# Optimization experiments

Measured on AMD Instinct MI355X. Metric: run time of the kernel, lower is better.

Reference implementation:

```python
import jax, jax.numpy as jnp
import numpy as np

B = 2048
NUM_GENES = 4096
# (stratum, n_terms, input_dim, output_dim, genes_per_term) leaves -> root
CFG = [(4, 256, 16, 20, 16), (3, 64, 144, 20, 64), (2, 16, 336, 77, 256), (1, 4, 1332, 308, 1024), (0, 1, 5328, 1229, 4096)]
EPS = 1e-5


def setup_inputs() -> dict:
    key = jax.random.key(0)
    ks = iter(jax.random.split(key, 64))
    inp = {"x": jax.random.uniform(next(ks), (B, NUM_GENES), dtype=jnp.float32)}
    sc = 0.05  # uniform init scale (original uses 0.001; scaled up for numerically robust baseline)
    for s, T, I, O, _ in CFG:
        inp[f"W{s}"] = jax.random.uniform(next(ks), (T, I, O), minval=-sc, maxval=sc, dtype=jnp.float32)
        inp[f"b{s}"] = jax.random.uniform(next(ks), (T, O), minval=-sc, maxval=sc, dtype=jnp.float32)
        inp[f"g{s}"] = jnp.ones((T, O), jnp.float32)   # BN weight
        inp[f"bb{s}"] = jnp.zeros((T, O), jnp.float32)  # BN bias
        inp[f"hw{s}"] = jax.random.uniform(next(ks), (T, O, 1), minval=-sc, maxval=sc, dtype=jnp.float32)
        inp[f"hb{s}"] = jnp.zeros((T, 1), jnp.float32)
    return inp


def _forward(x, W4, b4, g4, bb4, hw4, hb4, W3, b3, g3, bb3, hw3, hb3,
             W2, b2, g2, bb2, hw2, hb2, W1, b1, g1, bb1, hw1, hb1,
             W0, b0, g0, bb0, hw0, hb0):
    Bm = x.shape[0]
    params = [(W4, b4, g4, bb4, hw4, hb4), (W3, b3, g3, bb3, hw3, hb3),
              (W2, b2, g2, bb2, hw2, hb2), (W1, b1, g1, bb1, hw1, hb1),
              (W0, b0, g0, bb0, hw0, hb0)]
    act = None
    heads = []
    for (W, b, g, bb, hw, hb), (_, T, _, _, Gs) in zip(params, CFG):
        # gene states for each term: contiguous block gather == reshape
        genes = x.reshape(Bm, T, Gs)
        if act is None:
            inp = genes
        else:
            # concat 4 children outputs per parent, then gene states (children first, per _calculate_input_dim)
            inp = jnp.concatenate([act.reshape(Bm, T, -1), genes], axis=-1)
        # per-term Linear -> BatchNorm1d (training mode, biased var) -> Tanh, batched over terms
        h = jnp.einsum('bti,tio->bto', inp, W) + b
        mu = jnp.mean(h, axis=0)
        var = jnp.var(h, axis=0)
        act = jnp.tanh((h - mu) * jax.lax.rsqrt(var + EPS) * g + bb)
        # per-term linear head (output_size=1)
        heads.append(jnp.squeeze(jnp.einsum('bto,tos->bts', act, hw), -1) + hb[:, 0])
    # concat all per-term scalar outputs leaves->root; root prediction is heads[:, -1]
    return jnp.concatenate(heads, axis=1)


def reference(x, W4, b4, g4, bb4, hw4, hb4, W3, b3, g3, bb3, hw3, hb3,
              W2, b2, g2, bb2, hw2, hb2, W1, b1, g1, bb1, hw1, hb1,
              W0, b0, g0, bb0, hw0, hb0):
    return _forward(x, W4, b4, g4, bb4, hw4, hb4, W3, b3, g3, bb3, hw3, hb3,
                    W2, b2, g2, bb2, hw2, hb2, W1, b1, g1, bb1, hw1, hb1,
                    W0, b0, g0, bb0, hw0, hb0)
```

## Files before the change

### kernel.cpp

```cpp
#include <hip/hip_runtime.h>
#include <hip/hip_bf16.h>


#define BDIM 2048
#define OUTW 341

typedef __attribute__((ext_vector_type(8))) short short8;
typedef __attribute__((ext_vector_type(4))) float float4v;

static __device__ __forceinline__ unsigned short f2bf(float f) {
    union { float f; unsigned u; } c{f};
    unsigned r = c.u + 0x7FFF + ((c.u >> 16) & 1);
    return (unsigned short)(r >> 16);
}
static __device__ __forceinline__ float bf2f(unsigned short s) {
    union { unsigned u; float f; } c{(unsigned)s << 16};
    return c.f;
}

static __device__ __forceinline__ float fast_tanh(float x) {
    float ax = __builtin_fabsf(x);
    float e  = __builtin_amdgcn_exp2f(ax * 2.8853900817779268f);
    float r  = 1.f - 2.f * __builtin_amdgcn_rcpf(e + 1.f);
    return __builtin_copysignf(r, x);
}

static __device__ __forceinline__ void bn_ss(float sm, float sq, float g, float bb,
                                             float& scale, float& shift) {
    float mu = sm * (1.f / BDIM);
    float var = sq * (1.f / BDIM) - mu * mu;
    scale = rsqrtf(var + 1e-5f) * g;
    shift = bb - mu * scale;
}

static __device__ __forceinline__ void stage16(const void* g, void* ldsBase, int lane) {
#if __has_builtin(__builtin_amdgcn_global_load_lds)
    __builtin_amdgcn_global_load_lds(
        (const __attribute__((address_space(1))) unsigned int*)(uintptr_t)g,
        (__attribute__((address_space(3))) unsigned int*)(unsigned int)(uintptr_t)ldsBase,
        16, 0, 0);
#else
    *(uint4*)((char*)ldsBase + lane * 16) = *(const uint4*)g;
#endif
}

static __device__ __forceinline__ void cvt_w_body(const float* Wt, unsigned short* dst,
                                                  int I, int O, int Npad, int Kpad,
                                                  int i0, int o0, int tid) {
    __shared__ unsigned short tile[32][33];
    const int c = tid & 31, r0 = tid >> 5;
    #pragma unroll
    for (int rr = 0; rr < 4; rr++) {
        int i = i0 + r0 + rr * 8, o = o0 + c;
        float v = (i < I && o < O) ? Wt[(size_t)i * O + o] : 0.f;
        tile[r0 + rr * 8][c] = f2bf(v);
    }
    __syncthreads();
    #pragma unroll
    for (int rr = 0; rr < 4; rr++) {
        int o = o0 + r0 + rr * 8, k = i0 + c;
        if (o < Npad) dst[(size_t)o * Kpad + k] = tile[c][r0 + rr * 8];
    }
}

#define PACK_BLOCKS ((BDIM * 512 + BDIM * 24 + 255) / 256)
#define CVT_BLOCKS  2896
#define W0P1_BLOCKS (168 * 24)
__global__ __launch_bounds__(256) void pack_cvt(const float* __restrict__ x,
                                                unsigned short* __restrict__ ain0,
                                                unsigned short* __restrict__ ain1,
                                                const float* __restrict__ W4,
                                                const float* __restrict__ W3,
                                                const float* __restrict__ W2,
                                                const float* __restrict__ W1,
                                                const float* __restrict__ W0,
                                                unsigned short* __restrict__ wbt,
                                                float* __restrict__ acc) {
    int bid = blockIdx.x;
    if (bid < 20) {
        int idx = bid * 1024 + threadIdx.x * 4;
        *(float4*)(acc + idx) = make_float4(0.f, 0.f, 0.f, 0.f);
    }
    if (bid < PACK_BLOCKS) {
        const int MAIN = BDIM * 512;
        int i = bid * 256 + threadIdx.x;
        if (i < MAIN) {
            int b = i >> 9, j = i & 511;
            const float* xp = x + (size_t)b * 4096 + j * 8;
            float4 lo = *(const float4*)xp, hi = *(const float4*)(xp + 4);
            union { unsigned short u[8]; uint4 v4; uint2 v2[2]; } t;
            t.u[0] = f2bf(lo.x); t.u[1] = f2bf(lo.y); t.u[2] = f2bf(lo.z); t.u[3] = f2bf(lo.w);
            t.u[4] = f2bf(hi.x); t.u[5] = f2bf(hi.y); t.u[6] = f2bf(hi.z); t.u[7] = f2bf(hi.w);
            *(uint4*)(ain0 + (size_t)b * 5376 + 1232 + j * 8) = t.v4;
            int gi = j * 8, tt = gi >> 10, u = gi & 1023;
            unsigned short* d1 = ain1 + (size_t)b * 5376 + tt * 1344 + 308 + u;
            *(uint2*)d1 = t.v2[0];
            *(uint2*)(d1 + 4) = t.v2[1];
            return;
        }
        int zi = i - MAIN;
        const int ZU = BDIM * 12;
        if (zi < ZU) {
            int b = zi / 12, u = zi % 12;
            *(uint2*)(ain0 + (size_t)b * 5376 + 5328 + u * 4) = make_uint2(0u, 0u);
        } else if (zi < 2 * ZU) {
            zi -= ZU;
            int b = zi / 12, u = zi % 12, tt = u / 3, k = u % 3;
            *(uint2*)(ain1 + (size_t)b * 5376 + tt * 1344 + 1332 + k * 4) = make_uint2(0u, 0u);
        }
        return;
    }
    bid -= PACK_BLOCKS;
    if (bid >= CVT_BLOCKS) {
        bid -= CVT_BLOCKS;
        int bx = bid % 168, by = 16 + bid / 168;
        cvt_w_body(W0, wbt, 5328, 1229, 1280, 5376, bx * 32, by * 32, threadIdx.x);
        return;
    }
    const float* W; unsigned short* dst;
    int I, O, Npad, Kpad, gx, gy, local;
    if (bid < 256)       { W = W4; dst = wbt;           I = 16;   O = 20;  Npad = 20;  Kpad = 32;   gx = 1;  gy = 1;  local = bid; }
    else if (bid < 640)  { W = W3; dst = wbt + 163840;  I = 144;  O = 20;  Npad = 20;  Kpad = 192;  gx = 6;  gy = 1;  local = bid - 256; }
    else if (bid < 1216) { W = W2; dst = wbt + 409600;  I = 336;  O = 77;  Npad = 77;  Kpad = 384;  gx = 12; gy = 3;  local = bid - 640; }
    else                 { W = W1; dst = wbt + 882688;  I = 1332; O = 308; Npad = 320; Kpad = 1344; gx = 42; gy = 10; local = bid - 1216; }
    int per = gx * gy;
    int t = local / per, rem = local % per;
    int by = rem / gx, bx = rem % gx;
    cvt_w_body(W + (size_t)t * I * O, dst + (size_t)t * Npad * Kpad,
               I, O, Npad, Kpad, bx * 32, by * 32, threadIdx.x);
}

__global__ __launch_bounds__(256) void cvt_w(const float* __restrict__ W,
                                             unsigned short* __restrict__ WbT,
                                             int I, int O, int Npad, int Kpad) {
    cvt_w_body(W + (size_t)blockIdx.z * I * O, WbT + (size_t)blockIdx.z * Npad * Kpad,
               I, O, Npad, Kpad, blockIdx.x * 32, blockIdx.y * 32, threadIdx.x);
}

__global__ __launch_bounds__(256) void s4_stats(
    const unsigned short* __restrict__ xg,
    const unsigned short* __restrict__ wbt4,
    const float* __restrict__ b4,
    float* __restrict__ acc4)
{
    const int cg = blockIdx.x & 31;
    const int rc = blockIdx.x >> 5;
    const int t0 = cg * 8, b0 = rc * 64;
    const int tid = threadIdx.x;
    const int lane = tid & 63, w = tid >> 6;
    const int l15 = lane & 15, quad = lane >> 4;

    __shared__ __align__(16) unsigned short xs[64][168];

    #pragma unroll
    for (int j = 0; j < 4; j++) {
        int i = tid + j * 256;
        int r = i >> 4, gg = i & 15;
        *(uint4*)&xs[r][gg * 8] =
            *(const uint4*)(xg + (size_t)(b0 + r) * 5376 + t0 * 16 + gg * 8);
    }
    if (tid < 128) {
        int r = tid >> 1, gg = 16 + (tid & 1);
        *(uint4*)&xs[r][gg * 8] = make_uint4(0u, 0u, 0u, 0u);
    }
    __syncthreads();

    float4v acc[2][4][2];
    #pragma unroll
    for (int a = 0; a < 2; a++)
        #pragma unroll
        for (int b = 0; b < 4; b++)
            #pragma unroll
            for (int c = 0; c < 2; c++)
                acc[a][b][c] = (float4v){0.f, 0.f, 0.f, 0.f};

    #pragma unroll
    for (int ti = 0; ti < 2; ti++) {
        const int lt = w * 2 + ti;
        const int t = t0 + lt;
        short8 bf[2];
        #pragma unroll
        for (int nf = 0; nf < 2; nf++)
            bf[nf] = *(const short8*)(wbt4 + ((size_t)t * 20 + nf * 16 + l15) * 32 + quad * 8);
        #pragma unroll
        for (int mf = 0; mf < 4; mf++) {
            short8 a = *(const short8*)&xs[mf * 16 + l15][lt * 16 + quad * 8];
            #pragma unroll
            for (int nf = 0; nf < 2; nf++)
                acc[ti][mf][nf] = __builtin_amdgcn_mfma_f32_16x16x32_bf16(a, bf[nf], acc[ti][mf][nf], 0, 0, 0);
        }
    }

    #pragma unroll
    for (int ti = 0; ti < 2; ti++) {
        const int lt = w * 2 + ti;
        #pragma unroll
        for (int nf = 0; nf < 2; nf++) {
            const int o = nf * 16 + l15;
            const int col = (t0 + lt) * 20 + o;
            const bool valid = (o < 20);
            const float bias = valid ? b4[col] : 0.f;
            float s = 0.f, s2 = 0.f;
            #pragma unroll
            for (int mf = 0; mf < 4; mf++)
                #pragma unroll
                for (int r = 0; r < 4; r++) {
                    float v = acc[ti][mf][nf][r] + bias;
                    s += v; s2 += v * v;
                }
            s  += __shfl_xor(s, 16, 64);  s  += __shfl_xor(s, 32, 64);
            s2 += __shfl_xor(s2, 16, 64); s2 += __shfl_xor(s2, 32, 64);
            if (quad == 0 && valid) {
                atomicAdd(acc4 + col, s);
                atomicAdd(acc4 + 5120 + col, s2);
            }
        }
    }
}

__global__ __launch_bounds__(256) void s4s3_fused(
    const unsigned short* __restrict__ xg,
    const unsigned short* __restrict__ wbt4,
    const unsigned short* __restrict__ wbt3,
    const float* __restrict__ b4,
    const float* __restrict__ acc4,
    const float* __restrict__ g4,
    const float* __restrict__ bb4,
    const float* __restrict__ hw4,
    const float* __restrict__ hb4,
    const float* __restrict__ b3,
    unsigned short* __restrict__ h3,
    float* __restrict__ acc3,
    float* __restrict__ out)
{
    const int cg = blockIdx.x & 31;
    const int rc = blockIdx.x >> 5;
    const int t0 = cg * 8, b0 = rc * 64;
    const int tid = threadIdx.x;
    const int lane = tid & 63, w = tid >> 6;
    const int l15 = lane & 15, quad = lane >> 4;

    __shared__ __align__(16) unsigned short gs[64][152];
    __shared__ __align__(16) unsigned short as_[64][168];

    #pragma unroll
    for (int j = 0; j < 4; j++) {
        int i = tid + j * 256;
        int r = i >> 4, gg = i & 15;
        *(uint4*)&gs[r][gg * 8] =
            *(const uint4*)(xg + (size_t)(b0 + r) * 5376 + t0 * 16 + gg * 8);
    }
    if (tid < 128) {
        int r = tid >> 1, gg = 16 + (tid & 1);
        *(uint4*)&gs[r][gg * 8] = make_uint4(0u, 0u, 0u, 0u);
    }
    __syncthreads();

    float4v acc[2][4][2];
    #pragma unroll
    for (int a = 0; a < 2; a++)
        #pragma unroll
        for (int b = 0; b < 4; b++)
            #pragma unroll
            for (int c = 0; c < 2; c++)
                acc[a][b][c] = (float4v){0.f, 0.f, 0.f, 0.f};

    #pragma unroll
    for (int ti = 0; ti < 2; ti++) {
        const int lt = w * 2 + ti;
        const int t = t0 + lt;
        short8 bf[2];
        #pragma unroll
        for (int nf = 0; nf < 2; nf++)
            bf[nf] = *(const short8*)(wbt4 + ((size_t)t * 20 + nf * 16 + l15) * 32 + quad * 8);
        #pragma unroll
        for (int mf = 0; mf < 4; mf++) {
            short8 a = *(const short8*)&gs[mf * 16 + l15][lt * 16 + quad * 8];
            #pragma unroll
            for (int nf = 0; nf < 2; nf++)
                acc[ti][mf][nf] = __builtin_amdgcn_mfma_f32_16x16x32_bf16(a, bf[nf], acc[ti][mf][nf], 0, 0, 0);
        }
    }

    #pragma unroll
    for (int ti = 0; ti < 2; ti++) {
        const int lt = w * 2 + ti;
        const int t4 = t0 + lt;
        float hp[4][4];
        #pragma unroll
        for (int mf = 0; mf < 4; mf++)
            #pragma unroll
            for (int r = 0; r < 4; r++) hp[mf][r] = 0.f;
        #pragma unroll
        for (int nf = 0; nf < 2; nf++) {
            const int o = nf * 16 + l15;
            const int col = t4 * 20 + o;
            const bool valid = (o < 20);
            float scale = 0.f, shp = 0.f, hwv = 0.f;
            if (valid) {
                float sc, sh;
                bn_ss(acc4[col], acc4[5120 + col], g4[col], bb4[col], sc, sh);
                scale = sc;
                shp = b4[col] * sc + sh;
                hwv = hw4[col];
            }
            #pragma unroll
            for (int mf = 0; mf < 4; mf++)
                #pragma unroll
                for (int r = 0; r < 4; r++) {
                    float av = fast_tanh(acc[ti][mf][nf][r] * scale + shp);
                    if (valid)
                        as_[mf * 16 + quad * 4 + r][lt * 20 + o] = f2bf(av);
                    hp[mf][r] += av * hwv;
                }
        }
        const float hbv = hb4[t4];
        #pragma unroll
        for (int mf = 0; mf < 4; mf++)
            #pragma unroll
            for (int r = 0; r < 4; r++) {
                float v = hp[mf][r];
                v += __shfl_xor(v, 1, 64); v += __shfl_xor(v, 2, 64);
                v += __shfl_xor(v, 4, 64); v += __shfl_xor(v, 8, 64);
                if (l15 == 0)
                    out[(size_t)(b0 + mf * 16 + quad * 4 + r) * OUTW + t4] = v + hbv;
            }
    }
    __syncthreads();

    const int t3l = w & 1, mh = w >> 1;
    const int t3 = cg * 2 + t3l;
    float4v acc3r[2][2];
    #pragma unroll
    for (int a = 0; a < 2; a++)
        #pragma unroll
        for (int b = 0; b < 2; b++)
            acc3r[a][b] = (float4v){0.f, 0.f, 0.f, 0.f};

    #pragma unroll
    for (int ks = 0; ks < 5; ks++) {
        const int k = ks * 32 + quad * 8;
        short8 bf[2];
        #pragma unroll
        for (int nf = 0; nf < 2; nf++)
            bf[nf] = *(const short8*)(wbt3 + ((size_t)t3 * 20 + nf * 16 + l15) * 192 + ks * 32 + quad * 8);
        #pragma unroll
        for (int mf2 = 0; mf2 < 2; mf2++) {
            const int row = (mh * 2 + mf2) * 16 + l15;
            const unsigned short* ap = (k < 80) ? &as_[row][t3l * 80 + k]
                                                : &gs[row][t3l * 64 + (k - 80)];
            short8 a = *(const short8*)ap;
            #pragma unroll
            for (int nf = 0; nf < 2; nf++)
                acc3r[mf2][nf] = __builtin_amdgcn_mfma_f32_16x16x32_bf16(a, bf[nf], acc3r[mf2][nf], 0, 0, 0);
        }
    }

    float ss_[2], ss2_[2];
    #pragma unroll
    for (int nf = 0; nf < 2; nf++) { ss_[nf] = 0.f; ss2_[nf] = 0.f; }
    #pragma unroll
    for (int mf2 = 0; mf2 < 2; mf2++)
        #pragma unroll
        for (int nf = 0; nf < 2; nf++) {
            const int o = nf * 16 + l15;
            const int col = t3 * 20 + o;
            const bool valid = (o < 20);
            const float bias = valid ? b3[col] : 0.f;
            #pragma unroll
            for (int r = 0; r < 4; r++) {
                const int m = (mh * 2 + mf2) * 16 + quad * 4 + r;
                float v = acc3r[mf2][nf][r] + bias;
                if (valid)
                    h3[(size_t)(b0 + m) * 1280 + col] = f2bf(v);
                ss_[nf] += v; ss2_[nf] += v * v;
            }
        }
    #pragma unroll
    for (int nf = 0; nf < 2; nf++) {
        ss_[nf]  += __shfl_xor(ss_[nf], 16, 64);  ss_[nf]  += __shfl_xor(ss_[nf], 32, 64);
        ss2_[nf] += __shfl_xor(ss2_[nf], 16, 64); ss2_[nf] += __shfl_xor(ss2_[nf], 32, 64);
        const int o = nf * 16 + l15;
        if (quad == 0 && o < 20) {
            const int col = t3 * 20 + o;
            atomicAdd(acc3 + col, ss_[nf]);
            atomicAdd(acc3 + 1280 + col, ss2_[nf]);
        }
    }
}

template <int BN, int BK>
__global__ __launch_bounds__(256) void gemm_small(
    const unsigned short* __restrict__ actb,
    const unsigned short* __restrict__ xg,
    const unsigned short* __restrict__ WbT,
    const float* __restrict__ bias,
    unsigned short* __restrict__ h,
    float* __restrict__ acc,
    int T, int I, int O, int C, int Gs, int Kpad, int hstride, int TO)
{
    const int t  = blockIdx.z;
    const int b0 = blockIdx.y * 64;
    const int o0 = blockIdx.x * BN;
    const int tid = threadIdx.x;
    const int lane = tid & 63;
    const int w = tid >> 6;
    const int l15 = lane & 15;
    const int quad = lane >> 4;

    constexpr int NF = BN / 32;
    const int wm = (w & 1) * 32;
    const int wn = (w >> 1) * (BN / 2);

    __shared__ __align__(16) unsigned short As[64][BK + 8];
    __shared__ __align__(16) unsigned short Bs[BN][BK + 8];
    __shared__ float ldsS[2][BN], ldsS2[2][BN];

    float4v accr[2][NF];
    #pragma unroll
    for (int a = 0; a < 2; a++)
        #pragma unroll
        for (int b = 0; b < NF; b++)
            accr[a][b] = (float4v){0.f, 0.f, 0.f, 0.f};

    constexpr int GR = BK / 8;
    constexpr int AG = 64 * GR;
    constexpr int BG = BN * GR;
    const size_t actRow = (size_t)T * C;

    for (int k0 = 0; k0 < Kpad; k0 += BK) {
        #pragma unroll
        for (int g = tid; g < AG; g += 256) {
            const int r = g / GR, c8 = g % GR;
            const int k = k0 + c8 * 8;
            const int b = b0 + r;
            uint4 v;
            if (k + 8 <= C) {
                v = *(const uint4*)(actb + (size_t)b * actRow + (size_t)t * C + k);
            } else if (k >= I) {
                v = make_uint4(0u, 0u, 0u, 0u);
            } else {
                v = *(const uint4*)(xg + (size_t)b * 5376 + (size_t)t * Gs + (k - C));
            }
            *(uint4*)&As[r][c8 * 8] = v;
        }
        #pragma unroll
        for (int g = tid; g < BG; g += 256) {
            const int n = g / GR, c8 = g % GR;
            const int o = o0 + n;
            uint4 v = make_uint4(0u, 0u, 0u, 0u);
            if (o < O)
                v = *(const uint4*)(WbT + ((size_t)t * O + o) * Kpad + k0 + c8 * 8);
            *(uint4*)&Bs[n][c8 * 8] = v;
        }
        __syncthreads();
        #pragma unroll
        for (int ks = 0; ks < BK / 32; ks++) {
            const int koff = ks * 32 + quad * 8;
            short8 a0 = *(const short8*)&As[wm + l15][koff];
            short8 a1 = *(const short8*)&As[wm + 16 + l15][koff];
            #pragma unroll
            for (int fn = 0; fn < NF; fn++) {
                short8 bf = *(const short8*)&Bs[wn + fn * 16 + l15][koff];
                accr[0][fn] = __builtin_amdgcn_mfma_f32_16x16x32_bf16(a0, bf, accr[0][fn], 0, 0, 0);
                accr[1][fn] = __builtin_amdgcn_mfma_f32_16x16x32_bf16(a1, bf, accr[1][fn], 0, 0, 0);
            }
        }
        __syncthreads();
    }

    float csum[NF], csum2[NF];
    #pragma unroll
    for (int fn = 0; fn < NF; fn++) { csum[fn] = 0.f; csum2[fn] = 0.f; }
    #pragma unroll
    for (int fm = 0; fm < 2; fm++)
        #pragma unroll
        for (int fn = 0; fn < NF; fn++)
            #pragma unroll
            for (int r = 0; r < 4; r++) {
                int m = wm + fm * 16 + quad * 4 + r;
                int o = o0 + wn + fn * 16 + l15;
                if (o < O) {
                    float v = accr[fm][fn][r] + bias[t * O + o];
                    h[(size_t)(b0 + m) * hstride + (size_t)t * O + o] = f2bf(v);
                    csum[fn] += v; csum2[fn] += v * v;
                }
            }
    #pragma unroll
    for (int fn = 0; fn < NF; fn++) {
        csum[fn]  += __shfl_xor(csum[fn], 16, 64);
        csum[fn]  += __shfl_xor(csum[fn], 32, 64);
        csum2[fn] += __shfl_xor(csum2[fn], 16, 64);
        csum2[fn] += __shfl_xor(csum2[fn], 32, 64);
    }
    if (quad == 0) {
        #pragma unroll
        for (int fn = 0; fn < NF; fn++) {
            ldsS[w & 1][wn + fn * 16 + l15]  = csum[fn];
            ldsS2[w & 1][wn + fn * 16 + l15] = csum2[fn];
        }
    }
    __syncthreads();
    if (tid < BN && o0 + tid < O) {
        int col = t * O + o0 + tid;
        atomicAdd(acc + col,      ldsS[0][tid] + ldsS[1][tid]);
        atomicAdd(acc + TO + col, ldsS2[0][tid] + ldsS2[1][tid]);
    }
}

template <int BN>
__global__ __launch_bounds__(256) void gemm_split(
    const unsigned short* __restrict__ A,
    const unsigned short* __restrict__ WbT,
    float* __restrict__ partial,
    int aStride, int tStride, int Kpad, int Npad, int KS, int TNpad,
    int nTiles, int TKS)
{
    const int tid = threadIdx.x;
    const int lane = tid & 63, w = tid >> 6;
    const int l15 = lane & 15, quad = lane >> 4;

    const int id = blockIdx.x;
    const int c = id & 7;
    const int tmp = id >> 3;
    const int n = tmp % nTiles;
    const int q = tmp / nTiles;
    const int group = q * 8 + c;
    const int b0 = (group / TKS) * 128;
    const int rem = group % TKS;
    const int t = rem / KS;
    const int ksIdx = rem - t * KS;
    const int n0 = n * BN;

    __shared__ __align__(16) unsigned short As[2][128 * 32];
    __shared__ __align__(16) unsigned short Bs[2][BN * 32];

    const int S = Kpad >> 5;
    const int qb = S / KS, rb = S % KS;
    const int beg = ksIdx * qb + (ksIdx < rb ? ksIdx : rb);
    const int cnt = qb + (ksIdx < rb ? 1 : 0);

    constexpr int NF = BN / 32;
    const int wm = (w & 1) * 64;
    const int wn = (w >> 1) * (BN / 2);

    float4v acc[4][NF];
    #pragma unroll
    for (int a = 0; a < 4; a++)
        #pragma unroll
        for (int b = 0; b < NF; b++)
            acc[a][b] = (float4v){0.f, 0.f, 0.f, 0.f};

    const unsigned short* aSrc[2];
    int aOff[2];
    #pragma unroll
    for (int j = 0; j < 2; j++) {
        int s = (w * 2 + j) * 64 + lane;
        int r = s >> 2, kg = (s & 3) ^ ((r >> 1) & 3);
        aSrc[j] = A + (size_t)(b0 + r) * aStride + (size_t)t * tStride + kg * 8;
        aOff[j] = (w * 2 + j) * 512;
    }
    constexpr int BCALLS = (BN == 128) ? 2 : 1;
    const unsigned short* bSrc[BCALLS];
    int bOff[BCALLS];
    #pragma unroll
    for (int j = 0; j < BCALLS; j++) {
        int s = (w * BCALLS + j) * 64 + lane;
        int r = s >> 2, kg = (s & 3) ^ ((r >> 1) & 3);
        bSrc[j] = WbT + ((size_t)t * Npad + n0 + r) * Kpad + kg * 8;
        bOff[j] = (w * BCALLS + j) * 512;
    }

    {
        const int k0 = beg << 5;
        #pragma unroll
        for (int j = 0; j < 2; j++)      stage16(aSrc[j] + k0, &As[0][aOff[j]], lane);
        #pragma unroll
        for (int j = 0; j < BCALLS; j++) stage16(bSrc[j] + k0, &Bs[0][bOff[j]], lane);
    }

    for (int s = 0; s < cnt; s++) {
        const int cur = s & 1;
        __syncthreads();
        if (s + 1 < cnt) {
            const int k1 = (beg + s + 1) << 5;
            #pragma unroll
            for (int j = 0; j < 2; j++)      stage16(aSrc[j] + k1, &As[cur ^ 1][aOff[j]], lane);
            #pragma unroll
            for (int j = 0; j < BCALLS; j++) stage16(bSrc[j] + k1, &Bs[cur ^ 1][bOff[j]], lane);
        }
        short8 af[4];
        #pragma unroll
        for (int fm = 0; fm < 4; fm++) {
            int m = wm + fm * 16 + l15;
            int pos = quad ^ ((m >> 1) & 3);
            af[fm] = *(const short8*)&As[cur][(m * 4 + pos) * 8];
        }
        short8 bfr[NF];
        #pragma unroll
        for (int fn = 0; fn < NF; fn++) {
            int nn = wn + fn * 16 + l15;
            int pos = quad ^ ((nn >> 1) & 3);
            bfr[fn] = *(const short8*)&Bs[cur][(nn * 4 + pos) * 8];
        }
        #pragma unroll
        for (int fm = 0; fm < 4; fm++)
            #pragma unroll
            for (int fn = 0; fn < NF; fn++)
                acc[fm][fn] = __builtin_amdgcn_mfma_f32_16x16x32_bf16(af[fm], bfr[fn], acc[fm][fn], 0, 0, 0);
    }

    const size_t pBase = ((size_t)ksIdx * BDIM + b0) * TNpad + (size_t)t * Npad + n0;
    #pragma unroll
    for (int fm = 0; fm < 4; fm++)
        #pragma unroll
        for (int r = 0; r < 4; r++) {
            const int m = wm + fm * 16 + quad * 4 + r;
            float* prow = partial + pBase + (size_t)m * TNpad + wn;
            #pragma unroll
            for (int fn = 0; fn < NF; fn++)
                prow[fn * 16 + l15] = acc[fm][fn][r];
        }
}

__global__ __launch_bounds__(256) void reduce_bias_stats(
    const float* __restrict__ partial, const float* __restrict__ bias,
    unsigned short* __restrict__ h, float* __restrict__ acc,
    int T, int O, int Npad, int KS, int hstride, int TO)
{
    __shared__ float redS[4][64], redS2[4][64];
    const int colL = threadIdx.x & 63;
    const int cr = threadIdx.x >> 6;
    const int col = blockIdx.x * 64 + colL;
    const int chunk = blockIdx.y;
    float s = 0.f, s2 = 0.f;
    if (col < TO) {
        int t = col / O, o = col - t * O;
        const size_t TNpad = (size_t)T * Npad;
        const size_t pcol = (size_t)t * Npad + o;
        const float bv = bias[col];
        const int row0 = chunk * 128 + cr * 32;
        for (int r = 0; r < 32; r++) {
            const int row = row0 + r;
            const float* p = partial + (size_t)row * TNpad + pcol;
            float v = bv;
            for (int ks = 0; ks < KS; ks++) v += p[(size_t)ks * BDIM * TNpad];
            h[(size_t)row * hstride + col] = f2bf(v);
            s += v; s2 += v * v;
        }
    }
    redS[cr][colL] = s; redS2[cr][colL] = s2;
    __syncthreads();
    if (cr == 0 && col < TO) {
        float ts  = redS[0][colL] + redS[1][colL] + redS[2][colL] + redS[3][colL];
        float ts2 = redS2[0][colL] + redS2[1][colL] + redS2[2][colL] + redS2[3][colL];
        atomicAdd(acc + col, ts);
        atomicAdd(acc + TO + col, ts2);
    }
}

template <int GPT>
__global__ __launch_bounds__(256) void bn_tanh_head_vec(
    unsigned short* hact, const float* __restrict__ acc,
    const float* __restrict__ g, const float* __restrict__ bb,
    const float* __restrict__ hw, const float* __restrict__ hb,
    float* __restrict__ out,
    int T, int rowGran, int RPB, int hstride, int soff, int head_off)
{
    __shared__ float headAcc[256];
    const int tid = threadIdx.x;
    headAcc[tid] = 0.f;
    __syncthreads();
    const int b0 = blockIdx.x * RPB;

    uint2 hv[GPT];
    #pragma unroll
    for (int j = 0; j < GPT; j++) {
        int G = tid + j * 256;
        int r = G / rowGran, gg = G % rowGran;
        hv[j] = *(const uint2*)(hact + (size_t)(b0 + r) * hstride + gg * 4);
    }
    #pragma unroll
    for (int j = 0; j < GPT; j++) {
        int G = tid + j * 256;
        int r = G / rowGran, gg = G % rowGran;
        int c = gg * 4;
        float4 sm = *(const float4*)(acc + c);
        float4 sq = *(const float4*)(acc + soff + c);
        float4 gv = *(const float4*)(g + c);
        float4 bv = *(const float4*)(bb + c);
        float4 w4 = *(const float4*)(hw + c);
        float sc0, sh0, sc1, sh1, sc2, sh2, sc3, sh3;
        bn_ss(sm.x, sq.x, gv.x, bv.x, sc0, sh0);
        bn_ss(sm.y, sq.y, gv.y, bv.y, sc1, sh1);
        bn_ss(sm.z, sq.z, gv.z, bv.z, sc2, sh2);
        bn_ss(sm.w, sq.w, gv.w, bv.w, sc3, sh3);
        union { unsigned short u[4]; uint2 v; } iv, ov;
        iv.v = hv[j];
        float a0 = fast_tanh(bf2f(iv.u[0]) * sc0 + sh0);
        float a1 = fast_tanh(bf2f(iv.u[1]) * sc1 + sh1);
        float a2 = fast_tanh(bf2f(iv.u[2]) * sc2 + sh2);
        float a3 = fast_tanh(bf2f(iv.u[3]) * sc3 + sh3);
        ov.u[0] = f2bf(a0); ov.u[1] = f2bf(a1); ov.u[2] = f2bf(a2); ov.u[3] = f2bf(a3);
        *(uint2*)(hact + (size_t)(b0 + r) * hstride + c) = ov.v;
        float partial = a0 * w4.x + a1 * w4.y + a2 * w4.z + a3 * w4.w;
        int t = gg / 5;
        atomicAdd(&headAcc[r * T + t], partial);
    }
    __syncthreads();
    if (tid < RPB * T) {
        int r = tid / T, t = tid % T;
        out[(size_t)(b0 + r) * OUTW + head_off + t] = headAcc[tid] + hb[t];
    }
}

__global__ __launch_bounds__(256) void bn_tanh_head(
    const unsigned short* __restrict__ h, const float* __restrict__ acc,
    const float* __restrict__ g, const float* __restrict__ bb,
    const float* __restrict__ hw, const float* __restrict__ hb,
    unsigned short* __restrict__ actOut, float* __restrict__ out,
    int T, int O, int hstride, int aRow, int GT, int GS, int head_off, int TO)
{
    int wid  = (blockIdx.x * 256 + threadIdx.x) >> 6;
    int lane = threadIdx.x & 63;
    int b = wid / T;
    int t = wid % T;
    const size_t hbase = (size_t)b * hstride + (size_t)t * O;
    const size_t abase = (size_t)b * aRow + (size_t)(t / GT) * GS + (size_t)(t % GT) * O;
    float hsum = 0.f;
    for (int o = lane; o < O; o += 64) {
        int col = t * O + o;
        float sc, sh;
        bn_ss(acc[col], acc[TO + col], g[col], bb[col], sc, sh);
        float a = fast_tanh(bf2f(h[hbase + o]) * sc + sh);
        if (actOut) actOut[abase + o] = f2bf(a);
        hsum += a * hw[col];
    }
    #pragma unroll
    for (int off = 32; off > 0; off >>= 1) hsum += __shfl_down(hsum, off, 64);
    if (lane == 0) out[(size_t)b * OUTW + head_off + t] = hsum + hb[t];
}

extern "C" void kernel_launch(void* const* d_in, const int* in_sizes, int n_in,
                              void* d_out, int out_size, void* d_ws, size_t ws_size,
                              hipStream_t stream)
{
    const float* x = (const float*)d_in[0];
    float* out = (float*)d_out;
    char* ws = (char*)d_ws;

    unsigned short* wbt  = (unsigned short*)(ws);
    unsigned short* ain0 = (unsigned short*)(ws + 13762560);
    unsigned short* bufB = (unsigned short*)(ws + 56754176);
    unsigned short* ain1 = (unsigned short*)(ws + 61997056);
    unsigned short* bufC = (unsigned short*)(ws + 84017152);
    float*          accB = (float*)(ws + 89063424);
    float* partial = (float*)(ws + 35782656);
    unsigned short* xg = ain0 + 1232;
    float* acc4 = accB;
    float* acc3 = accB + 10240;
    float* acc2 = accB + 12800;
    float* acc1 = accB + 15264;
    float* acc0 = accB + 17728;

    const float* W4 = (const float*)d_in[1];  const float* b4 = (const float*)d_in[2];
    const float* g4 = (const float*)d_in[3];  const float* bb4 = (const float*)d_in[4];
    const float* hw4 = (const float*)d_in[5]; const float* hb4 = (const float*)d_in[6];
    const float* W3 = (const float*)d_in[7];  const float* b3 = (const float*)d_in[8];
    const float* g3 = (const float*)d_in[9];  const float* bb3 = (const float*)d_in[10];
    const float* hw3 = (const float*)d_in[11]; const float* hb3 = (const float*)d_in[12];
    const float* W2 = (const float*)d_in[13]; const float* b2 = (const float*)d_in[14];
    const float* g2 = (const float*)d_in[15]; const float* bb2 = (const float*)d_in[16];
    const float* hw2 = (const float*)d_in[17]; const float* hb2 = (const float*)d_in[18];
    const float* W1 = (const float*)d_in[19]; const float* b1 = (const float*)d_in[20];
    const float* g1 = (const float*)d_in[21]; const float* bb1 = (const float*)d_in[22];
    const float* hw1 = (const float*)d_in[23]; const float* hb1 = (const float*)d_in[24];
    const float* W0 = (const float*)d_in[25]; const float* b0_ = (const float*)d_in[26];
    const float* g0 = (const float*)d_in[27]; const float* bb0 = (const float*)d_in[28];
    const float* hw0 = (const float*)d_in[29]; const float* hb0 = (const float*)d_in[30];

    pack_cvt<<<PACK_BLOCKS + CVT_BLOCKS + W0P1_BLOCKS, 256, 0, stream>>>(
        x, ain0, ain1, W4, W3, W2, W1, W0, wbt, accB);

    s4_stats<<<1024, 256, 0, stream>>>(xg, wbt, b4, acc4);
    s4s3_fused<<<1024, 256, 0, stream>>>(xg, wbt, wbt + 163840, b4, acc4, g4, bb4,
                                         hw4, hb4, b3, bufB, acc3, out);

    bn_tanh_head_vec<5><<<BDIM / 4, 256, 0, stream>>>(bufB, acc3, g3, bb3, hw3, hb3,
                                                      out, 64, 320, 4, 1280, 1280, 256);

    gemm_small<96, 64><<<dim3(1, 32, 16), 256, 0, stream>>>(bufB, xg, wbt + 409600, b2, bufC,
                                                            acc2, 16, 336, 77, 80, 256, 384, 1232, 1232);
    bn_tanh_head<<<BDIM * 16 / 4, 256, 0, stream>>>(bufC, acc2, g2, bb2, hw2, hb2,
                                                    ain1, out, 16, 77, 1232, 5376, 4, 1344, 320, 1232);

    gemm_split<64><<<640, 256, 0, stream>>>(ain1, wbt + 882688, partial,
                                            5376, 1344, 1344, 320, 2, 1280, 5, 8);
    cvt_w<<<dim3(168, 16, 1), 256, 0, stream>>>(W0, wbt, 5328, 1229, 1280, 5376);
    reduce_bias_stats<<<dim3(20, 16), 256, 0, stream>>>(partial, b1, bufC, acc1,
                                                        4, 308, 320, 2, 1232, 1232);
    bn_tanh_head<<<BDIM * 4 / 4, 256, 0, stream>>>(bufC, acc1, g1, bb1, hw1, hb1,
                                                   ain0, out, 4, 308, 1232, 5376, 4, 0, 336, 1232);

    gemm_split<128><<<640, 256, 0, stream>>>(ain0, wbt, partial,
                                             5376, 0, 5376, 1280, 4, 1280, 10, 4);
    reduce_bias_stats<<<dim3(20, 16), 256, 0, stream>>>(partial, b0_, bufC, acc0,
                                                        1, 1229, 1280, 4, 1232, 1229);
    bn_tanh_head<<<BDIM / 4, 256, 0, stream>>>(bufC, acc0, g0, bb0, hw0, hb0,
                                               nullptr, out, 1, 1229, 1232, 1232, 1, 0, 340, 1229);
}
```

Baseline: 394.4 us.

## Fuse stratum-3 BN/tanh/head into stratum-2 GEMM and merge W0 convert with reduce

Stratum-3 batch-norm, tanh and per-term head are now applied inside the stratum-2 GEMM's A-tile load, so the separate elementwise pass and its read/write of the activation buffer are removed. The head sums go through shared-memory atomics and are written once per tile. The stratum-1 reduce and the late W0 bf16 conversion are merged into one launch to save a kernel launch and let the two run concurrently. The cost is redundant tanh work whenever the same activations are loaded by more than one block, plus LDS atomic contention.

```diff
diff --git a/kernel.cpp b/kernel.cpp
--- a/kernel.cpp
+++ b/kernel.cpp
@@ -128,13 +128,6 @@
     int by = rem / gx, bx = rem % gx;
     cvt_w_body(W + (size_t)t * I * O, dst + (size_t)t * Npad * Kpad,
                I, O, Npad, Kpad, bx * 32, by * 32, threadIdx.x);
-}
-
-__global__ __launch_bounds__(256) void cvt_w(const float* __restrict__ W,
-                                             unsigned short* __restrict__ WbT,
-                                             int I, int O, int Npad, int Kpad) {
-    cvt_w_body(W + (size_t)blockIdx.z * I * O, WbT + (size_t)blockIdx.z * Npad * Kpad,
-               I, O, Npad, Kpad, blockIdx.x * 32, blockIdx.y * 32, threadIdx.x);
 }
 
 __global__ __launch_bounds__(256) void s4_stats(
@@ -389,19 +382,23 @@
     }
 }
 
-template <int BN, int BK>
-__global__ __launch_bounds__(256) void gemm_small(
-    const unsigned short* __restrict__ actb,
+__global__ __launch_bounds__(256) void s2_fused(
+    const unsigned short* __restrict__ h3,
     const unsigned short* __restrict__ xg,
     const unsigned short* __restrict__ WbT,
-    const float* __restrict__ bias,
+    const float* __restrict__ acc3,
+    const float* __restrict__ g3, const float* __restrict__ bb3,
+    const float* __restrict__ hw3, const float* __restrict__ hb3,
+    const float* __restrict__ b2,
     unsigned short* __restrict__ h,
-    float* __restrict__ acc,
-    int T, int I, int O, int C, int Gs, int Kpad, int hstride, int TO)
+    float* __restrict__ acc2,
+    float* __restrict__ out)
 {
+    constexpr int BN = 96, BK = 64;
+    constexpr int I = 336, O = 77, C = 80, Gs = 256, Kpad = 384;
+    constexpr int hstride = 1232, TO = 1232;
     const int t  = blockIdx.z;
     const int b0 = blockIdx.y * 64;
-    const int o0 = blockIdx.x * BN;
     const int tid = threadIdx.x;
     const int lane = tid & 63;
     const int w = tid >> 6;
@@ -415,6 +412,17 @@
     __shared__ __align__(16) unsigned short As[64][BK + 8];
     __shared__ __align__(16) unsigned short Bs[BN][BK + 8];
     __shared__ float ldsS[2][BN], ldsS2[2][BN];
+    __shared__ float scL[80], shL[80], hwL[80];
+    __shared__ float headAcc[64][4];
+
+    if (tid < 80) {
+        int col = t * 80 + tid;
+        float sc, sh;
+        bn_ss(acc3[col], acc3[1280 + col], g3[col], bb3[col], sc, sh);
+        scL[tid] = sc; shL[tid] = sh; hwL[tid] = hw3[col];
+    }
+    headAcc[tid >> 2][tid & 3] = 0.f;
+    __syncthreads();
 
     float4v accr[2][NF];
     #pragma unroll
@@ -426,7 +434,6 @@
     constexpr int GR = BK / 8;
     constexpr int AG = 64 * GR;
     constexpr int BG = BN * GR;
-    const size_t actRow = (size_t)T * C;
 
     for (int k0 = 0; k0 < Kpad; k0 += BK) {
         #pragma unroll
@@ -434,23 +441,35 @@
             const int r = g / GR, c8 = g % GR;
             const int k = k0 + c8 * 8;
             const int b = b0 + r;
-            uint4 v;
             if (k + 8 <= C) {
-                v = *(const uint4*)(actb + (size_t)b * actRow + (size_t)t * C + k);
+                union { unsigned short u[8]; uint4 v; } hi_, ho;
+                hi_.v = *(const uint4*)(h3 + (size_t)b * 1280 + t * 80 + k);
+                const int tA = k / 20, tB = (k + 7) / 20;
+                float pA = 0.f, pB = 0.f;
+                #pragma unroll
+                for (int j = 0; j < 8; j++) {
+                    const int kk = k + j;
+                    float av = fast_tanh(bf2f(hi_.u[j]) * scL[kk] + shL[kk]);
+                    ho.u[j] = f2bf(av);
+                    float pr = av * hwL[kk];
+                    if (kk / 20 == tA) pA += pr; else pB += pr;
+                }
+                atomicAdd(&headAcc[r][tA], pA);
+                if (tB != tA) atomicAdd(&headAcc[r][tB], pB);
+                *(uint4*)&As[r][c8 * 8] = ho.v;
             } else if (k >= I) {
-                v = make_uint4(0u, 0u, 0u, 0u);
+                *(uint4*)&As[r][c8 * 8] = make_uint4(0u, 0u, 0u, 0u);
             } else {
-                v = *(const uint4*)(xg + (size_t)b * 5376 + (size_t)t * Gs + (k - C));
+                *(uint4*)&As[r][c8 * 8] =
+                    *(const uint4*)(xg + (size_t)b * 5376 + t * Gs + (k - C));
             }
-            *(uint4*)&As[r][c8 * 8] = v;
         }
         #pragma unroll
         for (int g = tid; g < BG; g += 256) {
             const int n = g / GR, c8 = g % GR;
-            const int o = o0 + n;
             uint4 v = make_uint4(0u, 0u, 0u, 0u);
-            if (o < O)
-                v = *(const uint4*)(WbT + ((size_t)t * O + o) * Kpad + k0 + c8 * 8);
+            if (n < O)
+                v = *(const uint4*)(WbT + ((size_t)t * O + n) * Kpad + k0 + c8 * 8);
             *(uint4*)&Bs[n][c8 * 8] = v;
         }
         __syncthreads();
@@ -469,6 +488,12 @@
         __syncthreads();
     }
 
+    {
+        const int r = tid >> 2, t3l = tid & 3;
+        const int t3 = t * 4 + t3l;
+        out[(size_t)(b0 + r) * OUTW + 256 + t3] = headAcc[r][t3l] + hb3[t3];
+    }
+
     float csum[NF], csum2[NF];
     #pragma unroll
     for (int fn = 0; fn < NF; fn++) { csum[fn] = 0.f; csum2[fn] = 0.f; }
@@ -479,9 +504,9 @@
             #pragma unroll
             for (int r = 0; r < 4; r++) {
                 int m = wm + fm * 16 + quad * 4 + r;
-                int o = o0 + wn + fn * 16 + l15;
+                int o = wn + fn * 16 + l15;
                 if (o < O) {
-                    float v = accr[fm][fn][r] + bias[t * O + o];
+                    float v = accr[fm][fn][r] + b2[t * O + o];
                     h[(size_t)(b0 + m) * hstride + (size_t)t * O + o] = f2bf(v);
                     csum[fn] += v; csum2[fn] += v * v;
                 }
@@ -501,10 +526,10 @@
         }
     }
     __syncthreads();
-    if (tid < BN && o0 + tid < O) {
-        int col = t * O + o0 + tid;
-        atomicAdd(acc + col,      ldsS[0][tid] + ldsS[1][tid]);
-        atomicAdd(acc + TO + col, ldsS2[0][tid] + ldsS2[1][tid]);
+    if (tid < BN && tid < O) {
+        int col = t * O + tid;
+        atomicAdd(acc2 + col,      ldsS[0][tid] + ldsS[1][tid]);
+        atomicAdd(acc2 + TO + col, ldsS2[0][tid] + ldsS2[1][tid]);
     }
 }
 
@@ -621,6 +646,50 @@
             for (int fn = 0; fn < NF; fn++)
                 prow[fn * 16 + l15] = acc[fm][fn][r];
         }
+}
+
+__global__ __launch_bounds__(256) void reduce1_cvtw0(
+    const float* __restrict__ partial, const float* __restrict__ bias,
+    unsigned short* __restrict__ h, float* __restrict__ acc,
+    const float* __restrict__ W0, unsigned short* __restrict__ wbt)
+{
+    const int bid = blockIdx.x;
+    if (bid >= 320) {
+        int local = bid - 320;
+        int bx = local % 168, by = local / 168;
+        cvt_w_body(W0, wbt, 5328, 1229, 1280, 5376, bx * 32, by * 32, threadIdx.x);
+        return;
+    }
+    constexpr int T = 4, O = 308, Npad = 320, KS = 2, hstride = 1232, TO = 1232;
+    __shared__ float redS[4][64], redS2[4][64];
+    const int colL = threadIdx.x & 63;
+    const int cr = threadIdx.x >> 6;
+    const int col = (bid % 20) * 64 + colL;
+    const int chunk = bid / 20;
+    float s = 0.f, s2 = 0.f;
+    if (col < TO) {
+        int t = col / O, o = col - t * O;
+        const size_t TNpad = (size_t)T * Npad;
+        const size_t pcol = (size_t)t * Npad + o;
+        const float bv = bias[col];
+        const int row0 = chunk * 128 + cr * 32;
+        for (int r = 0; r < 32; r++) {
+            const int row = row0 + r;
+            const float* p = partial + (size_t)row * TNpad + pcol;
+            float v = bv;
+            for (int ks = 0; ks < KS; ks++) v += p[(size_t)ks * BDIM * TNpad];
+            h[(size_t)row * hstride + col] = f2bf(v);
+            s += v; s2 += v * v;
+        }
+    }
+    redS[cr][colL] = s; redS2[cr][colL] = s2;
+    __syncthreads();
+    if (cr == 0 && col < TO) {
+        float ts  = redS[0][colL] + redS[1][colL] + redS[2][colL] + redS[3][colL];
+        float ts2 = redS2[0][colL] + redS2[1][colL] + redS2[2][colL] + redS2[3][colL];
+        atomicAdd(acc + col, ts);
+        atomicAdd(acc + TO + col, ts2);
+    }
 }
 
 __global__ __launch_bounds__(256) void reduce_bias_stats(
@@ -659,61 +728,6 @@
     }
 }
 
-template <int GPT>
-__global__ __launch_bounds__(256) void bn_tanh_head_vec(
-    unsigned short* hact, const float* __restrict__ acc,
-    const float* __restrict__ g, const float* __restrict__ bb,
-    const float* __restrict__ hw, const float* __restrict__ hb,
-    float* __restrict__ out,
-    int T, int rowGran, int RPB, int hstride, int soff, int head_off)
-{
-    __shared__ float headAcc[256];
-    const int tid = threadIdx.x;
-    headAcc[tid] = 0.f;
-    __syncthreads();
-    const int b0 = blockIdx.x * RPB;
-
-    uint2 hv[GPT];
-    #pragma unroll
-    for (int j = 0; j < GPT; j++) {
-        int G = tid + j * 256;
-        int r = G / rowGran, gg = G % rowGran;
-        hv[j] = *(const uint2*)(hact + (size_t)(b0 + r) * hstride + gg * 4);
-    }
-    #pragma unroll
-    for (int j = 0; j < GPT; j++) {
-        int G = tid + j * 256;
-        int r = G / rowGran, gg = G % rowGran;
-        int c = gg * 4;
-        float4 sm = *(const float4*)(acc + c);
-        float4 sq = *(const float4*)(acc + soff + c);
-        float4 gv = *(const float4*)(g + c);
-        float4 bv = *(const float4*)(bb + c);
-        float4 w4 = *(const float4*)(hw + c);
-        float sc0, sh0, sc1, sh1, sc2, sh2, sc3, sh3;
-        bn_ss(sm.x, sq.x, gv.x, bv.x, sc0, sh0);
-        bn_ss(sm.y, sq.y, gv.y, bv.y, sc1, sh1);
-        bn_ss(sm.z, sq.z, gv.z, bv.z, sc2, sh2);
-        bn_ss(sm.w, sq.w, gv.w, bv.w, sc3, sh3);
-        union { unsigned short u[4]; uint2 v; } iv, ov;
-        iv.v = hv[j];
-        float a0 = fast_tanh(bf2f(iv.u[0]) * sc0 + sh0);
-        float a1 = fast_tanh(bf2f(iv.u[1]) * sc1 + sh1);
-        float a2 = fast_tanh(bf2f(iv.u[2]) * sc2 + sh2);
-        float a3 = fast_tanh(bf2f(iv.u[3]) * sc3 + sh3);
-        ov.u[0] = f2bf(a0); ov.u[1] = f2bf(a1); ov.u[2] = f2bf(a2); ov.u[3] = f2bf(a3);
-        *(uint2*)(hact + (size_t)(b0 + r) * hstride + c) = ov.v;
-        float partial = a0 * w4.x + a1 * w4.y + a2 * w4.z + a3 * w4.w;
-        int t = gg / 5;
-        atomicAdd(&headAcc[r * T + t], partial);
-    }
-    __syncthreads();
-    if (tid < RPB * T) {
-        int r = tid / T, t = tid % T;
-        out[(size_t)(b0 + r) * OUTW + head_off + t] = headAcc[tid] + hb[t];
-    }
-}
-
 __global__ __launch_bounds__(256) void bn_tanh_head(
     const unsigned short* __restrict__ h, const float* __restrict__ acc,
     const float* __restrict__ g, const float* __restrict__ bb,
@@ -786,19 +800,15 @@
     s4s3_fused<<<1024, 256, 0, stream>>>(xg, wbt, wbt + 163840, b4, acc4, g4, bb4,
                                          hw4, hb4, b3, bufB, acc3, out);
 
-    bn_tanh_head_vec<5><<<BDIM / 4, 256, 0, stream>>>(bufB, acc3, g3, bb3, hw3, hb3,
-                                                      out, 64, 320, 4, 1280, 1280, 256);
-
-    gemm_small<96, 64><<<dim3(1, 32, 16), 256, 0, stream>>>(bufB, xg, wbt + 409600, b2, bufC,
-                                                            acc2, 16, 336, 77, 80, 256, 384, 1232, 1232);
+    s2_fused<<<dim3(1, 32, 16), 256, 0, stream>>>(bufB, xg, wbt + 409600, acc3,
+                                                  g3, bb3, hw3, hb3, b2,
+                                                  bufC, acc2, out);
     bn_tanh_head<<<BDIM * 16 / 4, 256, 0, stream>>>(bufC, acc2, g2, bb2, hw2, hb2,
                                                     ain1, out, 16, 77, 1232, 5376, 4, 1344, 320, 1232);
 
     gemm_split<64><<<640, 256, 0, stream>>>(ain1, wbt + 882688, partial,
                                             5376, 1344, 1344, 320, 2, 1280, 5, 8);
-    cvt_w<<<dim3(168, 16, 1), 256, 0, stream>>>(W0, wbt, 5328, 1229, 1280, 5376);
-    reduce_bias_stats<<<dim3(20, 16), 256, 0, stream>>>(partial, b1, bufC, acc1,
-                                                        4, 308, 320, 2, 1232, 1232);
+    reduce1_cvtw0<<<320 + 2688, 256, 0, stream>>>(partial, b1, bufC, acc1, W0, wbt);
     bn_tanh_head<<<BDIM * 4 / 4, 256, 0, stream>>>(bufC, acc1, g1, bb1, hw1, hb1,
                                                    ain0, out, 4, 308, 1232, 5376, 4, 0, 336, 1232);
 
```

Result: faster. 372.7 us (-5.5%).
